# Kernel optimization log

Hardware: AMD Instinct MI355X
Metric: run time of the kernel (lower is better)

## Reference

```python
import jax, jax.numpy as jnp
import numpy as np

CHUNK = 64  # mamba chunk size


def _ssd_chunk_scan(x, dt, A, Bs, Cs, R):
    """Exact chunked selective scan (mamba_chunk_scan_combined math, no D skip).
    x: [B,L,H,P] (H=K*R heads), dt: [B,L,H] (already softplus'd),
    A: [H], Bs/Cs: [B,L,K,N] groups (head h uses group h//R).
    Returns y: [B,L,H,P]."""
    Bsz, L, Hh, P = x.shape
    K, N = Bs.shape[2], Bs.shape[3]
    Nc = L // CHUNK
    # broadcast groups -> heads (head k*R+r uses group k)
    Bh = jnp.repeat(Bs, R, axis=2)  # [B,L,H,N]
    Ch = jnp.repeat(Cs, R, axis=2)
    xc = x.reshape(Bsz, Nc, CHUNK, Hh, P)
    dtc = dt.reshape(Bsz, Nc, CHUNK, Hh)
    Bc = Bh.reshape(Bsz, Nc, CHUNK, Hh, N)
    Cc = Ch.reshape(Bsz, Nc, CHUNK, Hh, N)
    dA = jnp.transpose(dtc, (0, 1, 3, 2)) * A[None, None, :, None]  # [B,Nc,H,Q]
    Acum = jnp.cumsum(dA, axis=-1)
    # intra-chunk decay matrix Lmat[i,j] = exp(sum_{j<s<=i} dA_s), lower-tri
    diff = Acum[..., :, None] - Acum[..., None, :]  # [B,Nc,H,Q,Q]
    tri = jnp.tril(jnp.ones((CHUNK, CHUNK), bool))
    Lmat = jnp.where(tri, jnp.exp(diff), 0.0)
    xdt = xc * dtc[..., None]  # dt enters as dt_j * B_j * x_j
    Y_diag = jnp.einsum('bcqhn,bcshn,bchqs,bcshp->bcqhp', Cc, Bc, Lmat, xdt)
    # chunk end states
    decay_last = jnp.exp(Acum[..., -1:] - Acum)  # [B,Nc,H,Q]
    states = jnp.einsum('bcqhn,bchq,bcqhp->bchpn', Bc, decay_last, xdt)
    chunk_decay = jnp.exp(Acum[..., -1])  # [B,Nc,H]
    def step(S, inp):
        cd, st = inp
        return cd[..., None, None] * S + st, S  # emit state BEFORE this chunk
    S0 = jnp.zeros((Bsz, Hh, P, N), x.dtype)
    _, prev = jax.lax.scan(step, S0, (jnp.moveaxis(chunk_decay, 1, 0), jnp.moveaxis(states, 1, 0)))
    prev = jnp.moveaxis(prev, 0, 1)  # [B,Nc,H,P,N]
    Y_off = jnp.einsum('bcqhn,bchpn,bchq->bcqhp', Cc, prev, jnp.exp(Acum))
    return (Y_diag + Y_off).reshape(Bsz, L, Hh, P)


def _forward(x, in_proj_w, conv_w, conv_b, x_proj_w, A_logs, Ds, dt_bias,
             out_norm_g, out_norm_b, out_proj_w):
    B, H, W, Dm = x.shape
    K, R = A_logs.shape
    P = Ds.shape[2]               # headdim
    d_inner = x_proj_w.shape[2]
    N = (x_proj_w.shape[1] - R) // 2
    L = H * W
    # in_proj + gate split
    xz = jnp.einsum('bhwc,dc->bhwd', x, in_proj_w)
    xi, z = jnp.split(xz, 2, axis=-1)
    z = jax.nn.gelu(z, approximate=False)
    # depthwise 3x3 conv (torch weight [d_inner,1,3,3] -> HWIO [3,3,1,d_inner])
    kern = jnp.transpose(conv_w, (2, 3, 1, 0))
    xi = jax.lax.conv_general_dilated(xi, kern, (1, 1), 'SAME',
            dimension_numbers=('NHWC', 'HWIO', 'NHWC'),
            feature_group_count=d_inner) + conv_b
    xi = jax.nn.gelu(xi, approximate=False)
    # cross2d scan: row-major, col-major, and their reverses
    x0 = xi.reshape(B, L, d_inner)
    x1 = jnp.transpose(xi, (0, 2, 1, 3)).reshape(B, L, d_inner)
    xs = jnp.stack([x0, x1, x0[:, ::-1], x1[:, ::-1]], axis=2)  # [B,L,K,d_inner]
    x_dbl = jnp.einsum('blkd,kcd->blkc', xs, x_proj_w)
    dts = x_dbl[..., :R].reshape(B, L, K * R)
    Bs = x_dbl[..., R:R + N]
    Cs = x_dbl[..., R + N:]
    xs_h = xs.reshape(B, L, K * R, P)
    A = -jnp.exp(A_logs.astype(jnp.float32)).reshape(K * R)
    Dmat = Ds.astype(jnp.float32).reshape(K * R, P)
    dt = jax.nn.softplus(dts + dt_bias.reshape(K * R))
    ys = _ssd_chunk_scan(xs_h, dt, A, Bs, Cs, R) + xs_h * Dmat  # D skip on raw x
    ys = ys.reshape(B, L, K, d_inner)
    # cross merge: invert each scan order, sum over K
    def unT(y):
        return jnp.transpose(y.reshape(B, W, H, d_inner), (0, 2, 1, 3)).reshape(B, L, d_inner)
    y = ys[:, :, 0] + ys[:, ::-1, 2] + unT(ys[:, :, 1]) + unT(ys[:, ::-1, 3])
    # out LayerNorm
    y = y.reshape(B, H, W, d_inner)
    mu = y.mean(-1, keepdims=True)
    var = y.var(-1, keepdims=True)
    y = (y - mu) / jnp.sqrt(var + 1e-5) * out_norm_g + out_norm_b
    y = y * z  # gating
    return jnp.einsum('bhwd,cd->bhwc', y, out_proj_w)


def setup_inputs() -> dict:
    key = jax.random.key(0)
    ks = jax.random.split(key, 10)
    B, H, W, Dm = 2, 64, 64, 192
    d_inner, K, R, N = 384, 4, 12, 64
    P = d_inner // R  # 32
    s = 0.02
    return {
        'x': jax.random.normal(ks[0], (B, H, W, Dm), jnp.float32),
        'in_proj_w': s * jax.random.normal(ks[1], (2 * d_inner, Dm), jnp.float32),
        'conv_w': s * jax.random.normal(ks[2], (d_inner, 1, 3, 3), jnp.float32),
        'conv_b': s * jax.random.normal(ks[3], (d_inner,), jnp.float32),
        'x_proj_w': s * jax.random.normal(ks[4], (K, R + 2 * N, d_inner), jnp.float32),
        'A_logs': 0.5 * jax.random.normal(ks[5], (K, R), jnp.float32),
        'Ds': jax.random.uniform(ks[6], (K, R, P), jnp.float32),
        'dt_bias': 0.1 * jax.random.uniform(ks[7], (K, R), jnp.float32),
        'out_norm_g': jnp.ones((d_inner,), jnp.float32),
        'out_norm_b': jnp.zeros((d_inner,), jnp.float32),
        'out_proj_w': s * jax.random.normal(ks[8], (Dm, d_inner), jnp.float32),
    }


def reference(x, in_proj_w, conv_w, conv_b, x_proj_w, A_logs, Ds, dt_bias,
              out_norm_g, out_norm_b, out_proj_w):
    return _forward(x, in_proj_w, conv_w, conv_b, x_proj_w, A_logs, Ds, dt_bias,
                    out_norm_g, out_norm_b, out_proj_w)
```

## Files before the change

kernel.cpp:

```cpp
#include <hip/hip_runtime.h>
#include <math.h>

#define DI 384

typedef __attribute__((ext_vector_type(8))) short bf8v;
typedef __attribute__((ext_vector_type(4))) float f4v;

__device__ __forceinline__ f4v mfma16(bf8v a, bf8v b, f4v c) {
  return __builtin_amdgcn_mfma_f32_16x16x32_bf16(a, b, c, 0, 0, 0);
}

__device__ __forceinline__ int trf(int l) { return ((l & 63) << 6) | (l >> 6); }
__device__ __forceinline__ int mapk(int k, int l) {
  if (k == 0) return l;
  if (k == 1) return trf(l);
  if (k == 2) return 4095 - l;
  return trf(4095 - l);
}
__device__ __forceinline__ float gelu_f(float x) {
  return 0.5f * x * (1.0f + erff(x * 0.7071067811865475f));
}
__device__ __forceinline__ float softplus_f(float x) {
  return (x > 20.0f) ? x : log1pf(expf(x));
}
__device__ __forceinline__ unsigned short f2bf(float f) {
  unsigned u = __float_as_uint(f);
  unsigned r = (u + 0x7fff + ((u >> 16) & 1)) >> 16;
  return (unsigned short)r;
}
__device__ __forceinline__ float bf2f(unsigned short h) {
  return __uint_as_float(((unsigned)h) << 16);
}
__device__ __forceinline__ unsigned short el16(uint2 v, int i) {
  unsigned w = (i < 2) ? v.x : v.y;
  return (unsigned short)((i & 1) ? (w >> 16) : (w & 0xffffu));
}
__device__ __forceinline__ int swz(int row, int col) {
  return (row << 6) + ((((col >> 3) ^ (row & 7)) << 3) | (col & 7));
}
__device__ __forceinline__ int foff(int row, int cb) {
  return (row << 6) + ((cb ^ (row & 7)) << 3);
}

__global__ __launch_bounds__(256) void k_cvt(const float* __restrict__ src,
                                             unsigned short* __restrict__ hi,
                                             unsigned short* __restrict__ lo, int n) {
  int i = blockIdx.x * 256 + threadIdx.x;
  if (i >= n) return;
  float v = src[i];
  unsigned short h = f2bf(v);
  hi[i] = h;
  lo[i] = f2bf(v - bf2f(h));
}

__global__ __launch_bounds__(256) void k_inproj(const unsigned short* __restrict__ Ahi,
                                                const unsigned short* __restrict__ Alo,
                                                const unsigned short* __restrict__ Whi,
                                                const unsigned short* __restrict__ Wlo,
                                                unsigned short* __restrict__ xr_hi,
                                                unsigned short* __restrict__ xr_lo,
                                                float* __restrict__ zg) {
  const int K = 192;
  __shared__ unsigned short Ah[4096], Al[4096], Bh[4096], Bl[4096];
  int tid = threadIdx.x;
  int lane = tid & 63, w = tid >> 6;
  int cl = lane & 15, kb = lane >> 4;
  int wm = w >> 1, wn = w & 1;
  int m0 = blockIdx.y * 64, n0 = blockIdx.x * 64;
  f4v acc[2][2];
  acc[0][0] = acc[0][1] = acc[1][0] = acc[1][1] = (f4v){0.f, 0.f, 0.f, 0.f};
  for (int k0 = 0; k0 < K; k0 += 64) {
#pragma unroll
    for (int u = 0; u < 2; ++u) {
      int unit = tid + u * 256;
      int row = unit >> 3, blk = unit & 7;
      int e = foff(row, blk);
      size_t ga = (size_t)(m0 + row) * K + k0 + blk * 8;
      size_t gb = (size_t)(n0 + row) * K + k0 + blk * 8;
      *(bf8v*)(Ah + e) = *(const bf8v*)(Ahi + ga);
      *(bf8v*)(Al + e) = *(const bf8v*)(Alo + ga);
      *(bf8v*)(Bh + e) = *(const bf8v*)(Whi + gb);
      *(bf8v*)(Bl + e) = *(const bf8v*)(Wlo + gb);
    }
    __syncthreads();
#pragma unroll
    for (int chunk = 0; chunk < 2; ++chunk) {
      int cb = chunk * 4 + kb;
      bf8v ah[2], al[2], bh[2], bl[2];
#pragma unroll
      for (int mi = 0; mi < 2; ++mi) {
        ah[mi] = *(const bf8v*)(Ah + foff(wm * 32 + mi * 16 + cl, cb));
        al[mi] = *(const bf8v*)(Al + foff(wm * 32 + mi * 16 + cl, cb));
      }
#pragma unroll
      for (int ni = 0; ni < 2; ++ni) {
        bh[ni] = *(const bf8v*)(Bh + foff(wn * 32 + ni * 16 + cl, cb));
        bl[ni] = *(const bf8v*)(Bl + foff(wn * 32 + ni * 16 + cl, cb));
      }
#pragma unroll
      for (int mi = 0; mi < 2; ++mi)
#pragma unroll
        for (int ni = 0; ni < 2; ++ni) {
          acc[mi][ni] = mfma16(ah[mi], bh[ni], acc[mi][ni]);
          acc[mi][ni] = mfma16(ah[mi], bl[ni], acc[mi][ni]);
          acc[mi][ni] = mfma16(al[mi], bh[ni], acc[mi][ni]);
        }
    }
    __syncthreads();
  }
#pragma unroll
  for (int mi = 0; mi < 2; ++mi)
#pragma unroll
    for (int ni = 0; ni < 2; ++ni)
#pragma unroll
      for (int i = 0; i < 4; ++i) {
        int m = m0 + wm * 32 + mi * 16 + kb * 4 + i;
        int n = n0 + wn * 32 + ni * 16 + cl;
        float v = acc[mi][ni][i];
        if (n < DI) {
          unsigned short hh = f2bf(v);
          xr_hi[(size_t)m * DI + n] = hh;
          xr_lo[(size_t)m * DI + n] = f2bf(v - bf2f(hh));
        } else {
          zg[(size_t)m * DI + (n - DI)] = gelu_f(v);
        }
      }
}

__global__ __launch_bounds__(256) void k_conv(const unsigned short* __restrict__ xrh,
                                              const unsigned short* __restrict__ xrl,
                                              const float* __restrict__ cw,
                                              const float* __restrict__ cb,
                                              unsigned short* __restrict__ xhi,
                                              unsigned short* __restrict__ xlo,
                                              unsigned short* __restrict__ xthi,
                                              unsigned short* __restrict__ xtlo) {
  int idx = blockIdx.x * 256 + threadIdx.x;
  int c = idx % DI;
  int lf = idx / DI;
  int b = lf >> 12;
  int l = lf & 4095;
  int h = l >> 6, w = l & 63;
  float acc = cb[c];
#pragma unroll
  for (int dh = -1; dh <= 1; ++dh) {
    int hh = h + dh;
    if ((unsigned)hh >= 64u) continue;
#pragma unroll
    for (int dw = -1; dw <= 1; ++dw) {
      int ww = w + dw;
      if ((unsigned)ww >= 64u) continue;
      size_t o = ((size_t)((b << 12) | (hh << 6) | ww)) * DI + c;
      acc += (bf2f(xrh[o]) + bf2f(xrl[o])) * cw[c * 9 + (dh + 1) * 3 + (dw + 1)];
    }
  }
  float g = gelu_f(acc);
  unsigned short hv = f2bf(g);
  unsigned short lv = f2bf(g - bf2f(hv));
  xhi[(size_t)idx] = hv;
  xlo[(size_t)idx] = lv;
  size_t tof = ((size_t)((b << 12) | trf(l))) * DI + c;
  xthi[tof] = hv;
  xtlo[tof] = lv;
}

__global__ __launch_bounds__(256) void k_xproj(const unsigned short* __restrict__ xhi,
                                               const unsigned short* __restrict__ xlo,
                                               const unsigned short* __restrict__ Whi,
                                               const unsigned short* __restrict__ Wlo,
                                               const float* __restrict__ dt_bias,
                                               float* __restrict__ dt_buf,
                                               unsigned short* __restrict__ Bhi,
                                               unsigned short* __restrict__ Blo,
                                               unsigned short* __restrict__ Chi,
                                               unsigned short* __restrict__ Clo) {
  const int K = DI, N = 140;
  int kdir = blockIdx.z;
  __shared__ unsigned short Ah[4096], Al[4096], Bh[4096], Bl[4096];
  __shared__ int rowbase[64];
  int tid = threadIdx.x;
  int lane = tid & 63, w = tid >> 6;
  int cl = lane & 15, kb = lane >> 4;
  int wm = w >> 1, wn = w & 1;
  int m0 = blockIdx.y * 64, n0 = blockIdx.x * 64;
  if (tid < 64) {
    int m = m0 + tid;
    int b = m >> 12, l = m & 4095;
    rowbase[tid] = (b << 12) + mapk(kdir, l);
  }
  const unsigned short* wkh = Whi + (size_t)kdir * N * K;
  const unsigned short* wkl = Wlo + (size_t)kdir * N * K;
  f4v acc[2][2];
  acc[0][0] = acc[0][1] = acc[1][0] = acc[1][1] = (f4v){0.f, 0.f, 0.f, 0.f};
  __syncthreads();
  for (int k0 = 0; k0 < K; k0 += 64) {
#pragma unroll
    for (int u = 0; u < 2; ++u) {
      int unit = tid + u * 256;
      int row = unit >> 3, blk = unit & 7;
      int e = foff(row, blk);
      size_t ga = (size_t)rowbase[row] * K + k0 + blk * 8;
      *(bf8v*)(Ah + e) = *(const bf8v*)(xhi + ga);
      *(bf8v*)(Al + e) = *(const bf8v*)(xlo + ga);
      int n = n0 + row;
      if (n < N) {
        size_t gb = (size_t)n * K + k0 + blk * 8;
        *(bf8v*)(Bh + e) = *(const bf8v*)(wkh + gb);
        *(bf8v*)(Bl + e) = *(const bf8v*)(wkl + gb);
      } else {
        bf8v z = {0, 0, 0, 0, 0, 0, 0, 0};
        *(bf8v*)(Bh + e) = z;
        *(bf8v*)(Bl + e) = z;
      }
    }
    __syncthreads();
#pragma unroll
    for (int chunk = 0; chunk < 2; ++chunk) {
      int cb = chunk * 4 + kb;
      bf8v ah[2], al[2], bh[2], bl[2];
#pragma unroll
      for (int mi = 0; mi < 2; ++mi) {
        ah[mi] = *(const bf8v*)(Ah + foff(wm * 32 + mi * 16 + cl, cb));
        al[mi] = *(const bf8v*)(Al + foff(wm * 32 + mi * 16 + cl, cb));
      }
#pragma unroll
      for (int ni = 0; ni < 2; ++ni) {
        bh[ni] = *(const bf8v*)(Bh + foff(wn * 32 + ni * 16 + cl, cb));
        bl[ni] = *(const bf8v*)(Bl + foff(wn * 32 + ni * 16 + cl, cb));
      }
#pragma unroll
      for (int mi = 0; mi < 2; ++mi)
#pragma unroll
        for (int ni = 0; ni < 2; ++ni) {
          acc[mi][ni] = mfma16(ah[mi], bh[ni], acc[mi][ni]);
          acc[mi][ni] = mfma16(ah[mi], bl[ni], acc[mi][ni]);
          acc[mi][ni] = mfma16(al[mi], bh[ni], acc[mi][ni]);
        }
    }
    __syncthreads();
  }
#pragma unroll
  for (int mi = 0; mi < 2; ++mi)
#pragma unroll
    for (int ni = 0; ni < 2; ++ni)
#pragma unroll
      for (int i = 0; i < 4; ++i) {
        int m = m0 + wm * 32 + mi * 16 + kb * 4 + i;
        int n = n0 + wn * 32 + ni * 16 + cl;
        if (n >= N) continue;
        float v = acc[mi][ni][i];
        int b = m >> 12, l = m & 4095;
        if (n < 12) {
          dt_buf[(((size_t)(b * 48 + kdir * 12 + n)) << 12) + l] =
              softplus_f(v + dt_bias[kdir * 12 + n]);
        } else if (n < 76) {
          size_t off = (((size_t)((b * 4 + kdir) << 12)) + l) * 64 + (n - 12);
          unsigned short hh = f2bf(v);
          Bhi[off] = hh;
          Blo[off] = f2bf(v - bf2f(hh));
        } else {
          size_t off = (((size_t)((b * 4 + kdir) << 12)) + l) * 64 + (n - 76);
          unsigned short hh = f2bf(v);
          Chi[off] = hh;
          Clo[off] = f2bf(v - bf2f(hh));
        }
      }
}

__global__ __launch_bounds__(256) void k_dtacum(const float* __restrict__ dt_buf,
                                                const float* __restrict__ A_logs,
                                                float* __restrict__ ac_buf,
                                                float* __restrict__ cdec) {
  int bh = blockIdx.y;
  int c = blockIdx.x * 4 + (threadIdx.x >> 6);
  int lane = threadIdx.x & 63;
  int h = bh % 48;
  size_t o = ((size_t)bh << 12) + c * 64 + lane;
  float dtv = dt_buf[o];
  float v = dtv * (-__expf(A_logs[h]));
#pragma unroll
  for (int off = 1; off < 64; off <<= 1) {
    float u = __shfl_up(v, off, 64);
    if (lane >= off) v += u;
  }
  ac_buf[o] = v;
  if (lane == 63) cdec[bh * 64 + c] = __expf(v);
}

__global__ __launch_bounds__(256) void k_states(const unsigned short* __restrict__ xhi,
                                                const unsigned short* __restrict__ xthi,
                                                const float* __restrict__ dt_buf,
                                                const float* __restrict__ ac_buf,
                                                const unsigned short* __restrict__ Bhi,
                                                unsigned short* __restrict__ Shi) {
  int c = blockIdx.x, k = blockIdx.y >> 1, g = blockIdx.y & 1, b = blockIdx.z;
  __shared__ unsigned short Bt_h[4096];
  __shared__ unsigned short xw_h[2048];
  int tid = threadIdx.x;
  int lane = tid & 63, w = tid >> 6;
  int cl = lane & 15, kb = lane >> 4;
  const unsigned short* xp = (k & 1) ? xthi : xhi;
  int pg = tid & 7, qq = tid >> 3;
  int h0_ = k * 12 + g * 6;
  uint2 xgA[2], xgB[2];
#pragma unroll
  for (int qp = 0; qp < 2; ++qp) {
    int i = c * 64 + qq * 2 + qp;
    if (k & 2) i = 4095 - i;
    xgA[qp] = *(const uint2*)(xp + ((size_t)((b << 12) + i)) * DI + (g * 6) * 32 + pg * 4);
  }
  size_t dto0 = (((size_t)(b * 48 + h0_)) << 12) + c * 64 + lane;
  float dtA = dt_buf[dto0];
  float acA = ac_buf[dto0];
  float dtB, acB;
  size_t Bbase = (((size_t)((b * 4 + k) << 12)) + c * 64) * 64;
  {
    int n = lane;
#pragma unroll
    for (int it = 0; it < 8; ++it) {
      int q0 = 2 * (w + it * 4);
      unsigned short h0 = Bhi[Bbase + (size_t)q0 * 64 + n];
      unsigned short h1 = Bhi[Bbase + (size_t)(q0 + 1) * 64 + n];
      *(unsigned int*)(Bt_h + swz(n, q0)) = (unsigned)h0 | ((unsigned)h1 << 16);
    }
  }
  for (int rr = 0; rr < 6; ++rr) {
    int r = g * 6 + rr;
    int h = k * 12 + r;
    float v = acA;
    float alast = __shfl(v, 63, 64);
    float wq = dtA * __expf(alast - v);
    float w0 = __shfl(wq, qq * 2, 64), w1 = __shfl(wq, qq * 2 + 1, 64);
    __syncthreads();
#pragma unroll
    for (int pi = 0; pi < 4; ++pi) {
      int p = pg * 4 + pi;
      unsigned short h0 = f2bf(bf2f(el16(xgA[0], pi)) * w0);
      unsigned short h1 = f2bf(bf2f(el16(xgA[1], pi)) * w1);
      *(unsigned int*)(xw_h + swz(p, qq * 2)) = (unsigned)h0 | ((unsigned)h1 << 16);
    }
    __syncthreads();
    if (rr < 5) {
#pragma unroll
      for (int qp = 0; qp < 2; ++qp) {
        int i = c * 64 + qq * 2 + qp;
        if (k & 2) i = 4095 - i;
        xgB[qp] = *(const uint2*)(xp + ((size_t)((b << 12) + i)) * DI + (r + 1) * 32 + pg * 4);
      }
      size_t dton = (((size_t)(b * 48 + h + 1)) << 12) + c * 64 + lane;
      dtB = dt_buf[dton];
      acB = ac_buf[dton];
    }
    f4v acc0 = {0.f, 0.f, 0.f, 0.f}, acc1 = {0.f, 0.f, 0.f, 0.f};
#pragma unroll
    for (int chunk = 0; chunk < 2; ++chunk) {
      int cb_ = chunk * 4 + kb;
      bf8v bh = *(const bf8v*)(Bt_h + foff(w * 16 + cl, cb_));
      bf8v a0h = *(const bf8v*)(xw_h + foff(cl, cb_));
      bf8v a1h = *(const bf8v*)(xw_h + foff(16 + cl, cb_));
      acc0 = mfma16(a0h, bh, acc0);
      acc1 = mfma16(a1h, bh, acc1);
    }
    size_t sbase = ((size_t)(b * 48 + h) * 64 + c) * 2048;
#pragma unroll
    for (int i = 0; i < 4; ++i) {
      int prow = kb * 4 + i;
      int n = w * 16 + cl;
      Shi[sbase + (size_t)prow * 64 + n] = f2bf(acc0[i]);
      Shi[sbase + (size_t)(16 + prow) * 64 + n] = f2bf(acc1[i]);
    }
    xgA[0] = xgB[0];
    xgA[1] = xgB[1];
    dtA = dtB;
    acA = acB;
  }
}

__global__ __launch_bounds__(256) void k_scan(unsigned short* __restrict__ Shi,
                                              const float* __restrict__ cdec) {
  int j = blockIdx.x;
  int bh = blockIdx.y;
  int tid = threadIdx.x;
  size_t base0 = (size_t)bh * 64 * 2048 + j * 256 + tid;
  float S = 0.0f;
  float nxt = bf2f(Shi[base0]);
  for (int c = 0; c < 64; ++c) {
    float cd = cdec[bh * 64 + c];
    size_t idx = base0 + (size_t)c * 2048;
    float tmp = nxt;
    if (c < 63) nxt = bf2f(Shi[idx + 2048]);
    Shi[idx] = f2bf(S);
    S = cd * S + tmp;
  }
}

__global__ __launch_bounds__(256) void k_out(const unsigned short* __restrict__ xhi,
                                             const unsigned short* __restrict__ xlo,
                                             const unsigned short* __restrict__ xthi,
                                             const unsigned short* __restrict__ xtlo,
                                             const float* __restrict__ dt_buf,
                                             const float* __restrict__ ac_buf,
                                             const unsigned short* __restrict__ Bhi,
                                             const unsigned short* __restrict__ Blo,
                                             const unsigned short* __restrict__ Chi,
                                             const unsigned short* __restrict__ Clo,
                                             const float* __restrict__ Ds,
                                             const unsigned short* __restrict__ Phi,
                                             float* __restrict__ ys) {
  int c = blockIdx.x, k = blockIdx.y >> 1, g = blockIdx.y & 1, b = blockIdx.z;
  __shared__ unsigned short C_h[4096], C_l[4096];
  __shared__ unsigned short G_h[4096];
  __shared__ unsigned short Xbuf[4096];
  unsigned short* X_h = Xbuf;
  unsigned short* X_l = Xbuf + 2048;
  int tid = threadIdx.x;
  int lane = tid & 63, w = tid >> 6;
  int cl = lane & 15, kb = lane >> 4;
  const unsigned short* xph = (k & 1) ? xthi : xhi;
  const unsigned short* xpl = (k & 1) ? xtlo : xlo;
  int pg = tid & 7, sq = tid >> 3;
  int h0_ = k * 12 + g * 6;
  uint2 xghA[2], xglA[2], xghB[2], xglB[2];
#pragma unroll
  for (int sp = 0; sp < 2; ++sp) {
    int i = c * 64 + sq * 2 + sp;
    if (k & 2) i = 4095 - i;
    size_t o = ((size_t)((b << 12) + i)) * DI + (g * 6) * 32 + pg * 4;
    xghA[sp] = *(const uint2*)(xph + o);
    xglA[sp] = *(const uint2*)(xpl + o);
  }
  bf8v pfA[2][2], pfB[2][2];
  {
    size_t pb = ((size_t)(b * 48 + h0_) * 64 + c) * 2048;
#pragma unroll
    for (int chunk = 0; chunk < 2; ++chunk) {
      int cb_ = chunk * 4 + kb;
      pfA[chunk][0] = *(const bf8v*)(Phi + pb + (size_t)cl * 64 + cb_ * 8);
      pfA[chunk][1] = *(const bf8v*)(Phi + pb + (size_t)(16 + cl) * 64 + cb_ * 8);
    }
  }
  size_t dto0 = (((size_t)(b * 48 + h0_)) << 12) + c * 64 + lane;
  float dtA = dt_buf[dto0];
  float vA = ac_buf[dto0];
  float dtB, vB;
  size_t base64 = (((size_t)((b * 4 + k) << 12)) + c * 64) * 64;
  {
    int n0 = (tid & 31) * 2;
    int qq = tid >> 5;
#pragma unroll
    for (int it = 0; it < 8; ++it) {
      int q = qq + it * 8;
      size_t off = base64 + (size_t)q * 64 + n0;
      int e = swz(q, n0);
      *(unsigned int*)(C_h + e) = *(const unsigned int*)(Chi + off);
      *(unsigned int*)(C_l + e) = *(const unsigned int*)(Clo + off);
      *(unsigned int*)(G_h + e) = *(const unsigned int*)(Bhi + off);
      *(unsigned int*)(Xbuf + e) = *(const unsigned int*)(Blo + off);
    }
  }
  __syncthreads();
  bf8v caf_h[2], caf_l[2];
#pragma unroll
  for (int chunk = 0; chunk < 2; ++chunk) {
    caf_h[chunk] = *(const bf8v*)(C_h + foff(w * 16 + cl, chunk * 4 + kb));
    caf_l[chunk] = *(const bf8v*)(C_l + foff(w * 16 + cl, chunk * 4 + kb));
  }
  f4v cbt[4];
#pragma unroll
  for (int St = 0; St < 4; ++St) cbt[St] = (f4v){0.f, 0.f, 0.f, 0.f};
#pragma unroll
  for (int St = 0; St < 4; ++St) {
    int srow = St * 16 + cl;
#pragma unroll
    for (int chunk = 0; chunk < 2; ++chunk) {
      bf8v bh = *(const bf8v*)(G_h + foff(srow, chunk * 4 + kb));
      bf8v bl = *(const bf8v*)(Xbuf + foff(srow, chunk * 4 + kb));
      cbt[St] = mfma16(caf_h[chunk], bh, cbt[St]);
      cbt[St] = mfma16(caf_h[chunk], bl, cbt[St]);
      cbt[St] = mfma16(caf_l[chunk], bh, cbt[St]);
    }
  }
  for (int rr = 0; rr < 6; ++rr) {
    int r = g * 6 + rr;
    int h = k * 12 + r;
    float dtv = dtA;
    float v = vA;
    float ea = __expf(v);
    __syncthreads();
#pragma unroll
    for (int pi = 0; pi < 4; ++pi) {
      int p = pg * 4 + pi;
      int e = swz(p, sq * 2);
      *(unsigned int*)(X_h + e) =
          (unsigned)el16(xghA[0], pi) | ((unsigned)el16(xghA[1], pi) << 16);
      *(unsigned int*)(X_l + e) =
          (unsigned)el16(xglA[0], pi) | ((unsigned)el16(xglA[1], pi) << 16);
    }
    float vq[4];
#pragma unroll
    for (int i = 0; i < 4; ++i) vq[i] = __shfl(v, w * 16 + kb * 4 + i, 64);
#pragma unroll
    for (int St = 0; St < 4; ++St) {
      int s = St * 16 + cl;
      float vs = __shfl(v, s, 64);
      float dts = __shfl(dtv, s, 64);
#pragma unroll
      for (int i = 0; i < 4; ++i) {
        int q = w * 16 + kb * 4 + i;
        float gv = (q >= s) ? cbt[St][i] * __expf(vq[i] - vs) * dts : 0.0f;
        G_h[swz(q, s)] = f2bf(gv);
      }
    }
    __syncthreads();
    if (rr < 5) {
#pragma unroll
      for (int sp = 0; sp < 2; ++sp) {
        int i = c * 64 + sq * 2 + sp;
        if (k & 2) i = 4095 - i;
        size_t o = ((size_t)((b << 12) + i)) * DI + (r + 1) * 32 + pg * 4;
        xghB[sp] = *(const uint2*)(xph + o);
        xglB[sp] = *(const uint2*)(xpl + o);
      }
      size_t pbn = ((size_t)(b * 48 + h + 1) * 64 + c) * 2048;
#pragma unroll
      for (int chunk = 0; chunk < 2; ++chunk) {
        int cb_ = chunk * 4 + kb;
        pfB[chunk][0] = *(const bf8v*)(Phi + pbn + (size_t)cl * 64 + cb_ * 8);
        pfB[chunk][1] = *(const bf8v*)(Phi + pbn + (size_t)(16 + cl) * 64 + cb_ * 8);
      }
      size_t dton = (((size_t)(b * 48 + h + 1)) << 12) + c * 64 + lane;
      dtB = dt_buf[dton];
      vB = ac_buf[dton];
    }
    f4v aD0 = {0.f, 0.f, 0.f, 0.f}, aD1 = aD0, aO0 = aD0, aO1 = aD0;
#pragma unroll
    for (int chunk = 0; chunk < 2; ++chunk) {
      int cb_ = chunk * 4 + kb;
      int qrow = w * 16 + cl;
      bf8v gh = *(const bf8v*)(G_h + foff(qrow, cb_));
      bf8v x0h = *(const bf8v*)(X_h + foff(cl, cb_));
      bf8v x0l = *(const bf8v*)(X_l + foff(cl, cb_));
      bf8v x1h = *(const bf8v*)(X_h + foff(16 + cl, cb_));
      bf8v x1l = *(const bf8v*)(X_l + foff(16 + cl, cb_));
      aD0 = mfma16(gh, x0h, aD0);
      aD0 = mfma16(gh, x0l, aD0);
      aD1 = mfma16(gh, x1h, aD1);
      aD1 = mfma16(gh, x1l, aD1);
      aO0 = mfma16(caf_h[chunk], pfA[chunk][0], aO0);
      aO0 = mfma16(caf_l[chunk], pfA[chunk][0], aO0);
      aO1 = mfma16(caf_h[chunk], pfA[chunk][1], aO1);
      aO1 = mfma16(caf_l[chunk], pfA[chunk][1], aO1);
    }
    float D0 = Ds[h * 32 + cl], D1 = Ds[h * 32 + 16 + cl];
    size_t ybase = ((size_t)((b * 4 + k) << 12) + c * 64) * DI + r * 32;
#pragma unroll
    for (int i = 0; i < 4; ++i) {
      int q = w * 16 + kb * 4 + i;
      float eaq = __shfl(ea, q, 64);
      int e0 = swz(cl, q), e1 = swz(16 + cl, q);
      float xv0 = bf2f(X_h[e0]) + bf2f(X_l[e0]);
      float xv1 = bf2f(X_h[e1]) + bf2f(X_l[e1]);
      ys[ybase + (size_t)q * DI + cl] = aD0[i] + eaq * aO0[i] + D0 * xv0;
      ys[ybase + (size_t)q * DI + 16 + cl] = aD1[i] + eaq * aO1[i] + D1 * xv1;
    }
#pragma unroll
    for (int chunk = 0; chunk < 2; ++chunk) {
      pfA[chunk][0] = pfB[chunk][0];
      pfA[chunk][1] = pfB[chunk][1];
    }
    xghA[0] = xghB[0]; xghA[1] = xghB[1];
    xglA[0] = xglB[0]; xglA[1] = xglB[1];
    dtA = dtB;
    vA = vB;
  }
}

__global__ __launch_bounds__(128) void k_ln(const float* __restrict__ ys,
                                            const float* __restrict__ zg,
                                            const float* __restrict__ gg,
                                            const float* __restrict__ bb,
                                            unsigned short* __restrict__ y2h,
                                            unsigned short* __restrict__ y2l) {
  int row = blockIdx.x;
  int b = row >> 12, l = row & 4095;
  int l1 = trf(l);
  int l2 = 4095 - l;
  int l3 = 4095 - l1;
  int tid = threadIdx.x;
  float v[3];
  size_t base = ((size_t)(b * 4)) << 12;
#pragma unroll
  for (int j = 0; j < 3; ++j) {
    int d = tid + j * 128;
    v[j] = ys[(base + l) * DI + d] + ys[(base + 4096 + l1) * DI + d] +
           ys[(base + 8192 + l2) * DI + d] + ys[(base + 12288 + l3) * DI + d];
  }
  __shared__ float red[2];
  float s = v[0] + v[1] + v[2];
#pragma unroll
  for (int off = 32; off > 0; off >>= 1) s += __shfl_down(s, off, 64);
  if ((tid & 63) == 0) red[tid >> 6] = s;
  __syncthreads();
  float mu = (red[0] + red[1]) * (1.0f / 384.0f);
  __syncthreads();
  float d2 = 0.0f;
#pragma unroll
  for (int j = 0; j < 3; ++j) {
    float dd = v[j] - mu;
    d2 += dd * dd;
  }
#pragma unroll
  for (int off = 32; off > 0; off >>= 1) d2 += __shfl_down(d2, off, 64);
  if ((tid & 63) == 0) red[tid >> 6] = d2;
  __syncthreads();
  float rstd = rsqrtf((red[0] + red[1]) * (1.0f / 384.0f) + 1e-5f);
#pragma unroll
  for (int j = 0; j < 3; ++j) {
    int d = tid + j * 128;
    float yv = (v[j] - mu) * rstd * gg[d] + bb[d];
    float o = yv * zg[(size_t)row * DI + d];
    unsigned short hh = f2bf(o);
    y2h[(size_t)row * DI + d] = hh;
    y2l[(size_t)row * DI + d] = f2bf(o - bf2f(hh));
  }
}

__global__ __launch_bounds__(256) void k_outproj(const unsigned short* __restrict__ Ahi,
                                                 const unsigned short* __restrict__ Alo,
                                                 const unsigned short* __restrict__ Whi,
                                                 const unsigned short* __restrict__ Wlo,
                                                 float* __restrict__ out) {
  const int K = DI, NO = 192;
  __shared__ unsigned short Ah[4096], Al[4096], Bh[4096], Bl[4096];
  int tid = threadIdx.x;
  int lane = tid & 63, w = tid >> 6;
  int cl = lane & 15, kb = lane >> 4;
  int wm = w >> 1, wn = w & 1;
  int m0 = blockIdx.y * 64, n0 = blockIdx.x * 64;
  f4v acc[2][2];
  acc[0][0] = acc[0][1] = acc[1][0] = acc[1][1] = (f4v){0.f, 0.f, 0.f, 0.f};
  for (int k0 = 0; k0 < K; k0 += 64) {
#pragma unroll
    for (int u = 0; u < 2; ++u) {
      int unit = tid + u * 256;
      int row = unit >> 3, blk = unit & 7;
      int e = foff(row, blk);
      size_t ga = (size_t)(m0 + row) * K + k0 + blk * 8;
      size_t gb = (size_t)(n0 + row) * K + k0 + blk * 8;
      *(bf8v*)(Ah + e) = *(const bf8v*)(Ahi + ga);
      *(bf8v*)(Al + e) = *(const bf8v*)(Alo + ga);
      *(bf8v*)(Bh + e) = *(const bf8v*)(Whi + gb);
      *(bf8v*)(Bl + e) = *(const bf8v*)(Wlo + gb);
    }
    __syncthreads();
#pragma unroll
    for (int chunk = 0; chunk < 2; ++chunk) {
      int cb = chunk * 4 + kb;
      bf8v ah[2], al[2], bh[2], bl[2];
#pragma unroll
      for (int mi = 0; mi < 2; ++mi) {
        ah[mi] = *(const bf8v*)(Ah + foff(wm * 32 + mi * 16 + cl, cb));
        al[mi] = *(const bf8v*)(Al + foff(wm * 32 + mi * 16 + cl, cb));
      }
#pragma unroll
      for (int ni = 0; ni < 2; ++ni) {
        bh[ni] = *(const bf8v*)(Bh + foff(wn * 32 + ni * 16 + cl, cb));
        bl[ni] = *(const bf8v*)(Bl + foff(wn * 32 + ni * 16 + cl, cb));
      }
#pragma unroll
      for (int mi = 0; mi < 2; ++mi)
#pragma unroll
        for (int ni = 0; ni < 2; ++ni) {
          acc[mi][ni] = mfma16(ah[mi], bh[ni], acc[mi][ni]);
          acc[mi][ni] = mfma16(ah[mi], bl[ni], acc[mi][ni]);
          acc[mi][ni] = mfma16(al[mi], bh[ni], acc[mi][ni]);
        }
    }
    __syncthreads();
  }
#pragma unroll
  for (int mi = 0; mi < 2; ++mi)
#pragma unroll
    for (int ni = 0; ni < 2; ++ni)
#pragma unroll
      for (int i = 0; i < 4; ++i) {
        int m = m0 + wm * 32 + mi * 16 + kb * 4 + i;
        int n = n0 + wn * 32 + ni * 16 + cl;
        out[(size_t)m * NO + n] = acc[mi][ni][i];
      }
}

extern "C" void kernel_launch(void* const* d_in, const int* in_sizes, int n_in,
                              void* d_out, int out_size, void* d_ws, size_t ws_size,
                              hipStream_t stream) {
  const float* x = (const float*)d_in[0];
  const float* in_proj_w = (const float*)d_in[1];
  const float* conv_w = (const float*)d_in[2];
  const float* conv_b = (const float*)d_in[3];
  const float* x_proj_w = (const float*)d_in[4];
  const float* A_logs = (const float*)d_in[5];
  const float* Ds = (const float*)d_in[6];
  const float* dt_bias = (const float*)d_in[7];
  const float* out_norm_g = (const float*)d_in[8];
  const float* out_norm_b = (const float*)d_in[9];
  const float* out_proj_w = (const float*)d_in[10];
  float* out = (float*)d_out;

  float* ws = (float*)d_ws;
  float* xi_raw = ws;
  float* zg = xi_raw + 3145728;
  float* dt_buf = zg + 3145728;
  float* ac_buf = dt_buf + 393216;
  float* cdec = ac_buf + 393216;
  float* ys = cdec + 6144;
  unsigned short* u16p = (unsigned short*)(ys + 12582912);
  unsigned short* Shi = u16p;    u16p += 12582912;
  unsigned short* xi_hi = u16p;  u16p += 3145728;
  unsigned short* xi_lo = u16p;  u16p += 3145728;
  unsigned short* x_hi = u16p;   u16p += 1572864;
  unsigned short* x_lo = u16p;   u16p += 1572864;
  unsigned short* xit_lo = u16p; u16p += 3145728;
  unsigned short* win_hi = u16p; u16p += 147456;
  unsigned short* win_lo = u16p; u16p += 147456;
  unsigned short* wxp_hi = u16p; u16p += 215040;
  unsigned short* wxp_lo = u16p; u16p += 215040;
  unsigned short* wout_hi = u16p; u16p += 73728;
  unsigned short* wout_lo = u16p; u16p += 73728;
  unsigned short* Bhi = u16p;    u16p += 2097152;
  unsigned short* Blo = u16p;    u16p += 2097152;
  unsigned short* Chi = u16p;    u16p += 2097152;
  unsigned short* Clo = u16p;    u16p += 2097152;
  unsigned short* xit_hi = x_hi;
  unsigned short* xr_hi = (unsigned short*)xi_raw;
  unsigned short* xr_lo = xr_hi + 3145728;
  unsigned short* y2h = xr_hi;
  unsigned short* y2l = y2h + 3145728;

  k_cvt<<<(1572864 + 255) / 256, 256, 0, stream>>>(x, x_hi, x_lo, 1572864);
  k_cvt<<<(147456 + 255) / 256, 256, 0, stream>>>(in_proj_w, win_hi, win_lo, 147456);
  k_cvt<<<(215040 + 255) / 256, 256, 0, stream>>>(x_proj_w, wxp_hi, wxp_lo, 215040);
  k_cvt<<<(73728 + 255) / 256, 256, 0, stream>>>(out_proj_w, wout_hi, wout_lo, 73728);

  k_inproj<<<dim3(12, 128), 256, 0, stream>>>(x_hi, x_lo, win_hi, win_lo, xr_hi, xr_lo, zg);
  k_conv<<<dim3(12288), 256, 0, stream>>>(xr_hi, xr_lo, conv_w, conv_b, xi_hi, xi_lo,
                                          xit_hi, xit_lo);
  k_xproj<<<dim3(3, 128, 4), 256, 0, stream>>>(xi_hi, xi_lo, wxp_hi, wxp_lo, dt_bias,
                                               dt_buf, Bhi, Blo, Chi, Clo);
  k_dtacum<<<dim3(16, 96), 256, 0, stream>>>(dt_buf, A_logs, ac_buf, cdec);
  k_states<<<dim3(64, 8, 2), 256, 0, stream>>>(xi_hi, xit_hi, dt_buf, ac_buf, Bhi, Shi);
  k_scan<<<dim3(8, 96), 256, 0, stream>>>(Shi, cdec);
  k_out<<<dim3(64, 8, 2), 256, 0, stream>>>(xi_hi, xi_lo, xit_hi, xit_lo, dt_buf,
                                            ac_buf, Bhi, Blo, Chi, Clo, Ds, Shi, ys);
  k_ln<<<dim3(8192), 128, 0, stream>>>(ys, zg, out_norm_g, out_norm_b, y2h, y2l);
  k_outproj<<<dim3(3, 128), 256, 0, stream>>>(y2h, y2l, wout_hi, wout_lo, out);
}
```

Baseline: 186.5 us.

## Fuse fp32-to-bf16 split conversion into GEMM loaders and double-buffer scan LDS

Removes the four standalone conversion kernels and instead converts fp32 inputs and weights into hi/lo bf16 pairs while staging tiles into shared memory in the in_proj, x_proj and out_proj GEMMs. This saves four launches plus a round trip of the converted tensors through global memory, at the price of redundant per-tile conversion work and wider fp32 global loads. The states and output kernels also double-buffer their per-head LDS tiles so one barrier per head iteration can be dropped. The output kernel additionally precomputes the shuffled exp values once per head instead of per element.

```diff
diff --git a/kernel.cpp b/kernel.cpp
--- a/kernel.cpp
+++ b/kernel.cpp
@@ -35,6 +35,15 @@
   unsigned w = (i < 2) ? v.x : v.y;
   return (unsigned short)((i & 1) ? (w >> 16) : (w & 0xffffu));
 }
+__device__ __forceinline__ void cvt8v(const float* __restrict__ p, bf8v& hv, bf8v& lv) {
+#pragma unroll
+  for (int i = 0; i < 8; ++i) {
+    float v = p[i];
+    unsigned short h = f2bf(v);
+    hv[i] = (short)h;
+    lv[i] = (short)f2bf(v - bf2f(h));
+  }
+}
 __device__ __forceinline__ int swz(int row, int col) {
   return (row << 6) + ((((col >> 3) ^ (row & 7)) << 3) | (col & 7));
 }
@@ -42,21 +51,8 @@
   return (row << 6) + ((cb ^ (row & 7)) << 3);
 }
 
-__global__ __launch_bounds__(256) void k_cvt(const float* __restrict__ src,
-                                             unsigned short* __restrict__ hi,
-                                             unsigned short* __restrict__ lo, int n) {
-  int i = blockIdx.x * 256 + threadIdx.x;
-  if (i >= n) return;
-  float v = src[i];
-  unsigned short h = f2bf(v);
-  hi[i] = h;
-  lo[i] = f2bf(v - bf2f(h));
-}
-
-__global__ __launch_bounds__(256) void k_inproj(const unsigned short* __restrict__ Ahi,
-                                                const unsigned short* __restrict__ Alo,
-                                                const unsigned short* __restrict__ Whi,
-                                                const unsigned short* __restrict__ Wlo,
+__global__ __launch_bounds__(256) void k_inproj(const float* __restrict__ x,
+                                                const float* __restrict__ wip,
                                                 unsigned short* __restrict__ xr_hi,
                                                 unsigned short* __restrict__ xr_lo,
                                                 float* __restrict__ zg) {
@@ -75,12 +71,13 @@
       int unit = tid + u * 256;
       int row = unit >> 3, blk = unit & 7;
       int e = foff(row, blk);
-      size_t ga = (size_t)(m0 + row) * K + k0 + blk * 8;
-      size_t gb = (size_t)(n0 + row) * K + k0 + blk * 8;
-      *(bf8v*)(Ah + e) = *(const bf8v*)(Ahi + ga);
-      *(bf8v*)(Al + e) = *(const bf8v*)(Alo + ga);
-      *(bf8v*)(Bh + e) = *(const bf8v*)(Whi + gb);
-      *(bf8v*)(Bl + e) = *(const bf8v*)(Wlo + gb);
+      bf8v hv, lv;
+      cvt8v(x + (size_t)(m0 + row) * K + k0 + blk * 8, hv, lv);
+      *(bf8v*)(Ah + e) = hv;
+      *(bf8v*)(Al + e) = lv;
+      cvt8v(wip + (size_t)(n0 + row) * K + k0 + blk * 8, hv, lv);
+      *(bf8v*)(Bh + e) = hv;
+      *(bf8v*)(Bl + e) = lv;
     }
     __syncthreads();
 #pragma unroll
@@ -166,8 +163,7 @@
 
 __global__ __launch_bounds__(256) void k_xproj(const unsigned short* __restrict__ xhi,
                                                const unsigned short* __restrict__ xlo,
-                                               const unsigned short* __restrict__ Whi,
-                                               const unsigned short* __restrict__ Wlo,
+                                               const float* __restrict__ wxp,
                                                const float* __restrict__ dt_bias,
                                                float* __restrict__ dt_buf,
                                                unsigned short* __restrict__ Bhi,
@@ -188,8 +184,7 @@
     int b = m >> 12, l = m & 4095;
     rowbase[tid] = (b << 12) + mapk(kdir, l);
   }
-  const unsigned short* wkh = Whi + (size_t)kdir * N * K;
-  const unsigned short* wkl = Wlo + (size_t)kdir * N * K;
+  const float* wk = wxp + (size_t)kdir * N * K;
   f4v acc[2][2];
   acc[0][0] = acc[0][1] = acc[1][0] = acc[1][1] = (f4v){0.f, 0.f, 0.f, 0.f};
   __syncthreads();
@@ -199,14 +194,15 @@
       int unit = tid + u * 256;
       int row = unit >> 3, blk = unit & 7;
       int e = foff(row, blk);
-      size_t ga = (size_t)rowbase[row] * K + k0 + blk * 8;
+      size_t ga = (size_t)rowbase[row] * DI + k0 + blk * 8;
       *(bf8v*)(Ah + e) = *(const bf8v*)(xhi + ga);
       *(bf8v*)(Al + e) = *(const bf8v*)(xlo + ga);
       int n = n0 + row;
       if (n < N) {
-        size_t gb = (size_t)n * K + k0 + blk * 8;
-        *(bf8v*)(Bh + e) = *(const bf8v*)(wkh + gb);
-        *(bf8v*)(Bl + e) = *(const bf8v*)(wkl + gb);
+        bf8v hv, lv;
+        cvt8v(wk + (size_t)n * K + k0 + blk * 8, hv, lv);
+        *(bf8v*)(Bh + e) = hv;
+        *(bf8v*)(Bl + e) = lv;
       } else {
         bf8v z = {0, 0, 0, 0, 0, 0, 0, 0};
         *(bf8v*)(Bh + e) = z;
@@ -295,7 +291,7 @@
                                                 unsigned short* __restrict__ Shi) {
   int c = blockIdx.x, k = blockIdx.y >> 1, g = blockIdx.y & 1, b = blockIdx.z;
   __shared__ unsigned short Bt_h[4096];
-  __shared__ unsigned short xw_h[2048];
+  __shared__ unsigned short xwb[2][2048];
   int tid = threadIdx.x;
   int lane = tid & 63, w = tid >> 6;
   int cl = lane & 15, kb = lane >> 4;
@@ -331,7 +327,7 @@
     float alast = __shfl(v, 63, 64);
     float wq = dtA * __expf(alast - v);
     float w0 = __shfl(wq, qq * 2, 64), w1 = __shfl(wq, qq * 2 + 1, 64);
-    __syncthreads();
+    unsigned short* xw_h = xwb[rr & 1];
 #pragma unroll
     for (int pi = 0; pi < 4; ++pi) {
       int p = pg * 4 + pi;
@@ -409,10 +405,8 @@
                                              float* __restrict__ ys) {
   int c = blockIdx.x, k = blockIdx.y >> 1, g = blockIdx.y & 1, b = blockIdx.z;
   __shared__ unsigned short C_h[4096], C_l[4096];
-  __shared__ unsigned short G_h[4096];
-  __shared__ unsigned short Xbuf[4096];
-  unsigned short* X_h = Xbuf;
-  unsigned short* X_l = Xbuf + 2048;
+  __shared__ unsigned short Gb[2][4096];
+  __shared__ unsigned short Xb[2][4096];
   int tid = threadIdx.x;
   int lane = tid & 63, w = tid >> 6;
   int cl = lane & 15, kb = lane >> 4;
@@ -454,8 +448,8 @@
       int e = swz(q, n0);
       *(unsigned int*)(C_h + e) = *(const unsigned int*)(Chi + off);
       *(unsigned int*)(C_l + e) = *(const unsigned int*)(Clo + off);
-      *(unsigned int*)(G_h + e) = *(const unsigned int*)(Bhi + off);
-      *(unsigned int*)(Xbuf + e) = *(const unsigned int*)(Blo + off);
+      *(unsigned int*)(Gb[0] + e) = *(const unsigned int*)(Bhi + off);
+      *(unsigned int*)(Gb[1] + e) = *(const unsigned int*)(Blo + off);
     }
   }
   __syncthreads();
@@ -473,20 +467,23 @@
     int srow = St * 16 + cl;
 #pragma unroll
     for (int chunk = 0; chunk < 2; ++chunk) {
-      bf8v bh = *(const bf8v*)(G_h + foff(srow, chunk * 4 + kb));
-      bf8v bl = *(const bf8v*)(Xbuf + foff(srow, chunk * 4 + kb));
+      bf8v bh = *(const bf8v*)(Gb[0] + foff(srow, chunk * 4 + kb));
+      bf8v bl = *(const bf8v*)(Gb[1] + foff(srow, chunk * 4 + kb));
       cbt[St] = mfma16(caf_h[chunk], bh, cbt[St]);
       cbt[St] = mfma16(caf_h[chunk], bl, cbt[St]);
       cbt[St] = mfma16(caf_l[chunk], bh, cbt[St]);
     }
   }
+  __syncthreads();
   for (int rr = 0; rr < 6; ++rr) {
     int r = g * 6 + rr;
     int h = k * 12 + r;
     float dtv = dtA;
     float v = vA;
     float ea = __expf(v);
-    __syncthreads();
+    unsigned short* Gc = Gb[rr & 1];
+    unsigned short* X_h = Xb[rr & 1];
+    unsigned short* X_l = Xb[rr & 1] + 2048;
 #pragma unroll
     for (int pi = 0; pi < 4; ++pi) {
       int p = pg * 4 + pi;
@@ -496,9 +493,12 @@
       *(unsigned int*)(X_l + e) =
           (unsigned)el16(xglA[0], pi) | ((unsigned)el16(xglA[1], pi) << 16);
     }
-    float vq[4];
-#pragma unroll
-    for (int i = 0; i < 4; ++i) vq[i] = __shfl(v, w * 16 + kb * 4 + i, 64);
+    float vq[4], evq[4];
+#pragma unroll
+    for (int i = 0; i < 4; ++i) {
+      vq[i] = __shfl(v, w * 16 + kb * 4 + i, 64);
+      evq[i] = __shfl(ea, w * 16 + kb * 4 + i, 64);
+    }
 #pragma unroll
     for (int St = 0; St < 4; ++St) {
       int s = St * 16 + cl;
@@ -508,7 +508,7 @@
       for (int i = 0; i < 4; ++i) {
         int q = w * 16 + kb * 4 + i;
         float gv = (q >= s) ? cbt[St][i] * __expf(vq[i] - vs) * dts : 0.0f;
-        G_h[swz(q, s)] = f2bf(gv);
+        Gc[swz(q, s)] = f2bf(gv);
       }
     }
     __syncthreads();
@@ -537,7 +537,7 @@
     for (int chunk = 0; chunk < 2; ++chunk) {
       int cb_ = chunk * 4 + kb;
       int qrow = w * 16 + cl;
-      bf8v gh = *(const bf8v*)(G_h + foff(qrow, cb_));
+      bf8v gh = *(const bf8v*)(Gc + foff(qrow, cb_));
       bf8v x0h = *(const bf8v*)(X_h + foff(cl, cb_));
       bf8v x0l = *(const bf8v*)(X_l + foff(cl, cb_));
       bf8v x1h = *(const bf8v*)(X_h + foff(16 + cl, cb_));
@@ -556,7 +556,7 @@
 #pragma unroll
     for (int i = 0; i < 4; ++i) {
       int q = w * 16 + kb * 4 + i;
-      float eaq = __shfl(ea, q, 64);
+      float eaq = evq[i];
       int e0 = swz(cl, q), e1 = swz(16 + cl, q);
       float xv0 = bf2f(X_h[e0]) + bf2f(X_l[e0]);
       float xv1 = bf2f(X_h[e1]) + bf2f(X_l[e1]);
@@ -627,8 +627,7 @@
 
 __global__ __launch_bounds__(256) void k_outproj(const unsigned short* __restrict__ Ahi,
                                                  const unsigned short* __restrict__ Alo,
-                                                 const unsigned short* __restrict__ Whi,
-                                                 const unsigned short* __restrict__ Wlo,
+                                                 const float* __restrict__ wop,
                                                  float* __restrict__ out) {
   const int K = DI, NO = 192;
   __shared__ unsigned short Ah[4096], Al[4096], Bh[4096], Bl[4096];
@@ -646,11 +645,12 @@
       int row = unit >> 3, blk = unit & 7;
       int e = foff(row, blk);
       size_t ga = (size_t)(m0 + row) * K + k0 + blk * 8;
-      size_t gb = (size_t)(n0 + row) * K + k0 + blk * 8;
       *(bf8v*)(Ah + e) = *(const bf8v*)(Ahi + ga);
       *(bf8v*)(Al + e) = *(const bf8v*)(Alo + ga);
-      *(bf8v*)(Bh + e) = *(const bf8v*)(Whi + gb);
-      *(bf8v*)(Bl + e) = *(const bf8v*)(Wlo + gb);
+      bf8v hv, lv;
+      cvt8v(wop + (size_t)(n0 + row) * K + k0 + blk * 8, hv, lv);
+      *(bf8v*)(Bh + e) = hv;
+      *(bf8v*)(Bl + e) = lv;
     }
     __syncthreads();
 #pragma unroll
@@ -717,34 +717,21 @@
   unsigned short* Shi = u16p;    u16p += 12582912;
   unsigned short* xi_hi = u16p;  u16p += 3145728;
   unsigned short* xi_lo = u16p;  u16p += 3145728;
-  unsigned short* x_hi = u16p;   u16p += 1572864;
-  unsigned short* x_lo = u16p;   u16p += 1572864;
+  unsigned short* xit_hi = u16p; u16p += 3145728;
   unsigned short* xit_lo = u16p; u16p += 3145728;
-  unsigned short* win_hi = u16p; u16p += 147456;
-  unsigned short* win_lo = u16p; u16p += 147456;
-  unsigned short* wxp_hi = u16p; u16p += 215040;
-  unsigned short* wxp_lo = u16p; u16p += 215040;
-  unsigned short* wout_hi = u16p; u16p += 73728;
-  unsigned short* wout_lo = u16p; u16p += 73728;
   unsigned short* Bhi = u16p;    u16p += 2097152;
   unsigned short* Blo = u16p;    u16p += 2097152;
   unsigned short* Chi = u16p;    u16p += 2097152;
   unsigned short* Clo = u16p;    u16p += 2097152;
-  unsigned short* xit_hi = x_hi;
   unsigned short* xr_hi = (unsigned short*)xi_raw;
   unsigned short* xr_lo = xr_hi + 3145728;
   unsigned short* y2h = xr_hi;
   unsigned short* y2l = y2h + 3145728;
 
-  k_cvt<<<(1572864 + 255) / 256, 256, 0, stream>>>(x, x_hi, x_lo, 1572864);
-  k_cvt<<<(147456 + 255) / 256, 256, 0, stream>>>(in_proj_w, win_hi, win_lo, 147456);
-  k_cvt<<<(215040 + 255) / 256, 256, 0, stream>>>(x_proj_w, wxp_hi, wxp_lo, 215040);
-  k_cvt<<<(73728 + 255) / 256, 256, 0, stream>>>(out_proj_w, wout_hi, wout_lo, 73728);
-
-  k_inproj<<<dim3(12, 128), 256, 0, stream>>>(x_hi, x_lo, win_hi, win_lo, xr_hi, xr_lo, zg);
+  k_inproj<<<dim3(12, 128), 256, 0, stream>>>(x, in_proj_w, xr_hi, xr_lo, zg);
   k_conv<<<dim3(12288), 256, 0, stream>>>(xr_hi, xr_lo, conv_w, conv_b, xi_hi, xi_lo,
                                           xit_hi, xit_lo);
-  k_xproj<<<dim3(3, 128, 4), 256, 0, stream>>>(xi_hi, xi_lo, wxp_hi, wxp_lo, dt_bias,
+  k_xproj<<<dim3(3, 128, 4), 256, 0, stream>>>(xi_hi, xi_lo, x_proj_w, dt_bias,
                                                dt_buf, Bhi, Blo, Chi, Clo);
   k_dtacum<<<dim3(16, 96), 256, 0, stream>>>(dt_buf, A_logs, ac_buf, cdec);
   k_states<<<dim3(64, 8, 2), 256, 0, stream>>>(xi_hi, xit_hi, dt_buf, ac_buf, Bhi, Shi);
@@ -752,5 +739,5 @@
   k_out<<<dim3(64, 8, 2), 256, 0, stream>>>(xi_hi, xi_lo, xit_hi, xit_lo, dt_buf,
                                             ac_buf, Bhi, Blo, Chi, Clo, Ds, Shi, ys);
   k_ln<<<dim3(8192), 128, 0, stream>>>(ys, zg, out_norm_g, out_norm_b, y2h, y2l);
-  k_outproj<<<dim3(3, 128), 256, 0, stream>>>(y2h, y2l, wout_hi, wout_lo, out);
-}
+  k_outproj<<<dim3(3, 128), 256, 0, stream>>>(y2h, y2l, out_proj_w, out);
+}
```

Result: faster. 179.1 us (-4.0%).
